# Performance work log

Measured on AMD Instinct MI355X. Metric: run time of the kernel, lower is better.

The kernel has to match this reference:

```python
import jax, jax.numpy as jnp
import numpy as np

B, C, H, W = 4, 256, 180, 180
N_BOX = 64


def _box_mask(gt_boxes, H, W):
    # gt_boxes: [B, N, 4] int32 = [lt_x, lt_y, rb_x, rb_y]
    # Original fills gt_mask[i, lt_y:rb_y, rb_x:lt_x] = 1 (x-slice is flipped).
    ys = jnp.arange(H)[:, None]            # [H,1]
    xs = jnp.arange(W)[None, :]            # [1,W]
    lt_x = gt_boxes[:, :, 0][:, :, None, None]
    lt_y = gt_boxes[:, :, 1][:, :, None, None]
    rb_x = gt_boxes[:, :, 2][:, :, None, None]
    rb_y = gt_boxes[:, :, 3][:, :, None, None]
    inside = (ys >= lt_y) & (ys < rb_y) & (xs >= rb_x) & (xs < lt_x)  # [B,N,H,W]
    return jnp.any(inside, axis=1)         # [B,H,W] bool


def setup_inputs() -> dict:
    key = jax.random.key(0)
    k1, k2, k3, k4, k5, k6 = jax.random.split(key, 6)
    inp = jax.random.normal(k1, (B, C, H, W), dtype=jnp.float32)
    tgt = jax.random.normal(k2, (B, C, H, W), dtype=jnp.float32)
    # Build boxes with flipped-x convention: lt_x > rb_x, lt_y < rb_y.
    x2 = jax.random.randint(k3, (B, N_BOX), 0, W - 50)
    bw = jax.random.randint(k4, (B, N_BOX), 5, 45)
    y1 = jax.random.randint(k5, (B, N_BOX), 0, H - 50)
    bh = jax.random.randint(k6, (B, N_BOX), 5, 45)
    gt_boxes = jnp.stack([x2 + bw, y1, x2, y1 + bh], axis=-1).astype(jnp.int32)
    return {"input": inp, "target": tgt, "gt_boxes": gt_boxes}


def reference(input, target, gt_boxes):
    b, c, h, w = input.shape
    mask = _box_mask(gt_boxes, h, w)                        # [B,H,W]
    x = jnp.transpose(input, (0, 2, 3, 1))                  # [B,H,W,C]
    t = jnp.transpose(target, (0, 2, 3, 1))
    positives = jnp.any(t != 0, axis=-1).astype(x.dtype) * mask.astype(x.dtype)
    pos_normalizer = jnp.sum(positives)
    reg_weights = positives / pos_normalizer                # [B,H,W]
    # masked weighted MSE; zero weights make non-positive pixels contribute 0,
    # matching the original's boolean-index gather.
    t = jnp.where(jnp.isnan(t), x, t)
    loss = 0.5 * (x - t) ** 2 * reg_weights[..., None]      # [B,H,W,C]
    imitation_loss = jnp.sum(jnp.mean(loss, axis=-1)) / b
    return imitation_loss
```

## Files before the change

### kernel.cpp

```cpp
#include <hip/hip_runtime.h>
#include <hip/hip_bf16.h>

#define B_     4
#define C_     256
#define H_     180
#define W_     180
#define NBOX   64
#define HW_    (H_ * W_)
#define GROUPS (HW_ / 4)
#define GTILES 32
#define PTILES 127
#define KCH    16
#define CPC    16
#define NBLK   (PTILES * B_)

#define WMASK_OFF 0
#define PSUM_OFF  (B_ * HW_)
#define PNZ_OFF   (PSUM_OFF + KCH * B_ * GROUPS * 16)
#define ACC_OFF   (PNZ_OFF + KCH * B_ * GROUPS * 4)
#define WS_NEED   (ACC_OFF + 8)

__global__ __launch_bounds__(256) void mfl_mask(
    const int* __restrict__ boxes,
    unsigned char* __restrict__ wmask)
{
    const int tid = threadIdx.x;
    const int bx  = blockIdx.x;
    const int b   = blockIdx.y;

    __shared__ int sbox[NBOX * 4];
    sbox[tid] = boxes[b * NBOX * 4 + tid];
    __syncthreads();

    const int hw = bx * 256 + tid;
    if (hw < HW_) {
        const int h = hw / W_, w = hw - (hw / W_) * W_;
        int msk = 0;
        #pragma unroll 8
        for (int n = 0; n < NBOX; ++n) {
            const int ltx = sbox[n * 4 + 0];
            const int lty = sbox[n * 4 + 1];
            const int rbx = sbox[n * 4 + 2];
            const int rby = sbox[n * 4 + 3];
            msk |= ((h >= lty) & (h < rby) & (w >= rbx) & (w < ltx));
        }
        wmask[b * HW_ + hw] = (unsigned char)msk;
    }
}

__global__ __launch_bounds__(256, 8) void mfl_stream(
    const float4* __restrict__ x4,
    const float4* __restrict__ t4,
    const unsigned char* __restrict__ wmask,
    float4* __restrict__ psum,
    unsigned int* __restrict__ pnz)
{
    const int g = blockIdx.x * 256 + threadIdx.x;
    if (g >= GROUPS) return;
    const int k = blockIdx.y;
    const int b = blockIdx.z;

    const uchar4 m4 = *(const uchar4*)(wmask + b * HW_ + 4 * g);
    if ((m4.x | m4.y | m4.z | m4.w) == 0) return;

    const size_t fbase = ((size_t)(b * C_ + k * CPC)) * GROUPS + g;
    const float4* xp = x4 + fbase;
    const float4* tp = t4 + fbase;

    float a0 = 0.f, a1 = 0.f, a2 = 0.f, a3 = 0.f;
    int   n0 = 0, n1 = 0, n2 = 0, n3 = 0;

    #pragma unroll 4
    for (int c = 0; c < CPC; ++c) {
        const float4 tv = tp[(size_t)c * GROUPS];
        const float4 xv = xp[(size_t)c * GROUPS];
        n0 |= (tv.x != 0.f); n1 |= (tv.y != 0.f);
        n2 |= (tv.z != 0.f); n3 |= (tv.w != 0.f);
        float d0 = xv.x - tv.x, d1 = xv.y - tv.y;
        float d2 = xv.z - tv.z, d3 = xv.w - tv.w;
        float s0 = 0.5f * d0 * d0, s1 = 0.5f * d1 * d1;
        float s2 = 0.5f * d2 * d2, s3 = 0.5f * d3 * d3;
        if (isnan(tv.x)) s0 = 0.f;  if (isnan(tv.y)) s1 = 0.f;
        if (isnan(tv.z)) s2 = 0.f;  if (isnan(tv.w)) s3 = 0.f;
        a0 += s0; a1 += s1; a2 += s2; a3 += s3;
    }

    const size_t o = ((size_t)(k * B_ + b)) * GROUPS + g;
    psum[o] = make_float4(a0, a1, a2, a3);
    pnz[o]  = (unsigned int)n0 | ((unsigned int)n1 << 8)
            | ((unsigned int)n2 << 16) | ((unsigned int)n3 << 24);
}

__global__ __launch_bounds__(256) void mfl_gate(
    const float* __restrict__ psumf,
    const unsigned char* __restrict__ pnzb,
    const unsigned char* __restrict__ wmask,
    float* __restrict__ ws_sum,
    unsigned int* __restrict__ ws_cnt)
{
    const int tid = threadIdx.x;
    const int bx  = blockIdx.x;
    const int b   = blockIdx.y;
    const int hw  = bx * 256 + tid;

    float s = 0.f;
    int   nz = 0, msk = 0;
    if (hw < HW_) {
        msk = wmask[b * HW_ + hw];
        if (msk) {
            const int g = hw >> 2, e = hw & 3;
            #pragma unroll
            for (int k = 0; k < KCH; ++k) {
                const size_t o = ((size_t)(k * B_ + b)) * GROUPS + g;
                s  += psumf[o * 4 + e];
                nz |= pnzb[o * 4 + e];
            }
        }
    }
    const bool ok = msk && nz;
    float sc = ok ? s : 0.f;
    int   cc = ok ? 1 : 0;

    #pragma unroll
    for (int off = 32; off > 0; off >>= 1) {
        sc += __shfl_down(sc, off, 64);
        cc += __shfl_down(cc, off, 64);
    }
    __shared__ float ws[4];
    __shared__ int   wc[4];
    if ((tid & 63) == 0) { ws[tid >> 6] = sc; wc[tid >> 6] = cc; }
    __syncthreads();
    if (tid == 0) {
        const float S  = ws[0] + ws[1] + ws[2] + ws[3];
        const int   Cn = wc[0] + wc[1] + wc[2] + wc[3];
        if (S != 0.f) atomicAdd(ws_sum, S);
        if (Cn != 0)  atomicAdd(ws_cnt, (unsigned int)Cn);
    }
}

__global__ void mfl_final(const float* ws_sum, const unsigned int* ws_cnt,
                          float* out)
{
    out[0] = ws_sum[0] / ((float)ws_cnt[0] * (float)C_ * (float)B_);
}

__global__ __launch_bounds__(256) void mfl_fallback(
    const float* __restrict__ x, const float* __restrict__ t,
    const int* __restrict__ boxes, float* ws_sum, unsigned int* ws_cnt)
{
    const int p = blockIdx.x * blockDim.x + threadIdx.x;
    float s = 0.0f; int cnt = 0;
    if (p < B_ * HW_) {
        const int b = p / HW_, hw = p - b * HW_;
        const int h = hw / W_, w = hw - h * W_;
        bool mask = false;
        const int* bb = boxes + b * NBOX * 4;
        for (int n = 0; n < NBOX; ++n) {
            mask |= ((h >= bb[n*4+1]) & (h < bb[n*4+3]) & (w >= bb[n*4+2]) & (w < bb[n*4+0]));
        }
        if (mask) {
            const float* xp = x + (size_t)b * C_ * HW_ + hw;
            const float* tp = t + (size_t)b * C_ * HW_ + hw;
            bool anynz = false;
            for (int c = 0; c < C_; ++c) {
                const float tv = tp[(size_t)c * HW_], xv = xp[(size_t)c * HW_];
                anynz |= (tv != 0.0f);
                const float d = xv - tv;
                float term = 0.5f * d * d;
                if (isnan(tv)) term = 0.0f;
                s += term;
            }
            if (anynz) cnt = 1; else s = 0.0f;
        }
    }
    for (int off = 32; off > 0; off >>= 1) {
        s += __shfl_down(s, off, 64); cnt += __shfl_down(cnt, off, 64);
    }
    __shared__ float ssum[4]; __shared__ int scnt[4];
    if ((threadIdx.x & 63) == 0) { ssum[threadIdx.x >> 6] = s; scnt[threadIdx.x >> 6] = cnt; }
    __syncthreads();
    if (threadIdx.x == 0) {
        const float S = ssum[0]+ssum[1]+ssum[2]+ssum[3];
        const int Cn = scnt[0]+scnt[1]+scnt[2]+scnt[3];
        if (S != 0.0f) atomicAdd(ws_sum, S);
        if (Cn != 0) atomicAdd(ws_cnt, (unsigned int)Cn);
    }
}

extern "C" void kernel_launch(void* const* d_in, const int* in_sizes, int n_in,
                              void* d_out, int out_size, void* d_ws, size_t ws_size,
                              hipStream_t stream)
{
    const float* x     = (const float*)d_in[0];
    const float* t     = (const float*)d_in[1];
    const int*   boxes = (const int*)d_in[2];
    float* out = (float*)d_out;
    char*  ws  = (char*)d_ws;

    if (ws_size < (size_t)WS_NEED) {
        float* ws_sum = (float*)ws;
        unsigned int* ws_cnt = (unsigned int*)(ws + 4);
        hipMemsetAsync(d_ws, 0, 8, stream);
        mfl_fallback<<<(B_ * HW_ + 255) / 256, 256, 0, stream>>>(x, t, boxes, ws_sum, ws_cnt);
        mfl_final<<<1, 1, 0, stream>>>(ws_sum, ws_cnt, out);
        return;
    }

    unsigned char* wmask  = (unsigned char*)(ws + WMASK_OFF);
    float4*        psum   = (float4*)(ws + PSUM_OFF);
    unsigned int*  pnz    = (unsigned int*)(ws + PNZ_OFF);
    float*         ws_sum = (float*)(ws + ACC_OFF);
    unsigned int*  ws_cnt = (unsigned int*)(ws + ACC_OFF + 4);

    hipMemsetAsync(ws + ACC_OFF, 0, 8, stream);

    dim3 gm(PTILES, B_);
    mfl_mask<<<gm, 256, 0, stream>>>(boxes, wmask);

    dim3 ga(GTILES, KCH, B_);
    mfl_stream<<<ga, 256, 0, stream>>>((const float4*)x, (const float4*)t,
                                       wmask, psum, pnz);

    dim3 gb(PTILES, B_);
    mfl_gate<<<gb, 256, 0, stream>>>((const float*)psum,
                                     (const unsigned char*)pnz,
                                     wmask, ws_sum, ws_cnt);

    mfl_final<<<1, 1, 0, stream>>>(ws_sum, ws_cnt, out);
}
```

Before: 61.98 us.

## Rewrite streaming kernel with batched loads and drop per-pixel mask skip

Replaces the streaming reduction kernel with one where each thread handles two float4 pixel groups and issues eight target and eight input loads per step before computing, with a scheduling barrier to keep the loads in flight together. The per-group mask check is removed, so every pixel is streamed. The channel split drops from 16 to 8 chunks, giving 32 channels per block, and the gate kernel sums fewer partials. The aim is more memory-level parallelism and fewer divergent early exits, at the cost of reading data under masked-out pixels that was skipped before.

Measured after the change: 69.57 us. +12.3%, slower.

```diff
diff --git a/kernel.cpp b/kernel.cpp
--- a/kernel.cpp
+++ b/kernel.cpp
@@ -8,11 +8,11 @@
 #define NBOX   64
 #define HW_    (H_ * W_)
 #define GROUPS (HW_ / 4)
-#define GTILES 32
+#define WGRP   512
+#define SEGS   ((GROUPS + WGRP - 1) / WGRP)
+#define KCH    8
+#define NC     (C_ / KCH)
 #define PTILES 127
-#define KCH    16
-#define CPC    16
-#define NBLK   (PTILES * B_)
 
 #define WMASK_OFF 0
 #define PSUM_OFF  (B_ * HW_)
@@ -48,47 +48,82 @@
     }
 }
 
-__global__ __launch_bounds__(256, 8) void mfl_stream(
+__global__ __launch_bounds__(256) void mfl_stream2(
     const float4* __restrict__ x4,
     const float4* __restrict__ t4,
-    const unsigned char* __restrict__ wmask,
     float4* __restrict__ psum,
     unsigned int* __restrict__ pnz)
 {
-    const int g = blockIdx.x * 256 + threadIdx.x;
-    if (g >= GROUPS) return;
-    const int k = blockIdx.y;
-    const int b = blockIdx.z;
-
-    const uchar4 m4 = *(const uchar4*)(wmask + b * HW_ + 4 * g);
-    if ((m4.x | m4.y | m4.z | m4.w) == 0) return;
-
-    const size_t fbase = ((size_t)(b * C_ + k * CPC)) * GROUPS + g;
-    const float4* xp = x4 + fbase;
-    const float4* tp = t4 + fbase;
-
-    float a0 = 0.f, a1 = 0.f, a2 = 0.f, a3 = 0.f;
-    int   n0 = 0, n1 = 0, n2 = 0, n3 = 0;
-
-    #pragma unroll 4
-    for (int c = 0; c < CPC; ++c) {
-        const float4 tv = tp[(size_t)c * GROUPS];
-        const float4 xv = xp[(size_t)c * GROUPS];
-        n0 |= (tv.x != 0.f); n1 |= (tv.y != 0.f);
-        n2 |= (tv.z != 0.f); n3 |= (tv.w != 0.f);
-        float d0 = xv.x - tv.x, d1 = xv.y - tv.y;
-        float d2 = xv.z - tv.z, d3 = xv.w - tv.w;
-        float s0 = 0.5f * d0 * d0, s1 = 0.5f * d1 * d1;
-        float s2 = 0.5f * d2 * d2, s3 = 0.5f * d3 * d3;
-        if (isnan(tv.x)) s0 = 0.f;  if (isnan(tv.y)) s1 = 0.f;
-        if (isnan(tv.z)) s2 = 0.f;  if (isnan(tv.w)) s3 = 0.f;
-        a0 += s0; a1 += s1; a2 += s2; a3 += s3;
-    }
-
-    const size_t o = ((size_t)(k * B_ + b)) * GROUPS + g;
-    psum[o] = make_float4(a0, a1, a2, a3);
-    pnz[o]  = (unsigned int)n0 | ((unsigned int)n1 << 8)
-            | ((unsigned int)n2 << 16) | ((unsigned int)n3 << 24);
+    const int tid  = threadIdx.x;
+    const int lane = tid & 63;
+    const int wid  = tid >> 6;
+    const int seg  = blockIdx.x;
+    const int k    = blockIdx.y;
+    const int b    = blockIdx.z;
+
+    const int g0 = seg * WGRP + wid * 128 + lane;
+    const int g1 = g0 + 64;
+    const bool v0 = g0 < GROUPS, v1 = g1 < GROUPS;
+    const int cg0 = v0 ? g0 : GROUPS - 1;
+    const int cg1 = v1 ? g1 : GROUPS - 1;
+
+    const size_t base = (size_t)(b * C_ + k * NC) * GROUPS;
+
+    float4 s0 = make_float4(0.f, 0.f, 0.f, 0.f);
+    float4 s1 = make_float4(0.f, 0.f, 0.f, 0.f);
+    float4 z0 = make_float4(0.f, 0.f, 0.f, 0.f);
+    float4 z1 = make_float4(0.f, 0.f, 0.f, 0.f);
+
+    for (int cb = 0; cb < NC; cb += 4) {
+        float4 T[8], X[8];
+        #pragma unroll
+        for (int j = 0; j < 4; ++j) {
+            const size_t rb = base + (size_t)(cb + j) * GROUPS;
+            T[2 * j]     = t4[rb + cg0];
+            T[2 * j + 1] = t4[rb + cg1];
+        }
+        #pragma unroll
+        for (int j = 0; j < 4; ++j) {
+            const size_t rb = base + (size_t)(cb + j) * GROUPS;
+            X[2 * j]     = x4[rb + cg0];
+            X[2 * j + 1] = x4[rb + cg1];
+        }
+        __builtin_amdgcn_sched_barrier(0);
+        #pragma unroll
+        for (int j = 0; j < 8; ++j) {
+            const float4 tv = T[j];
+            const float4 xv = X[j];
+            float4& s = (j & 1) ? s1 : s0;
+            float4& z = (j & 1) ? z1 : z0;
+            z.x += (tv.x != 0.f) ? 1.f : 0.f;
+            z.y += (tv.y != 0.f) ? 1.f : 0.f;
+            z.z += (tv.z != 0.f) ? 1.f : 0.f;
+            z.w += (tv.w != 0.f) ? 1.f : 0.f;
+            float d0 = xv.x - tv.x, d1 = xv.y - tv.y;
+            float d2 = xv.z - tv.z, d3 = xv.w - tv.w;
+            float m0 = 0.5f * d0 * d0, m1 = 0.5f * d1 * d1;
+            float m2 = 0.5f * d2 * d2, m3 = 0.5f * d3 * d3;
+            if (isnan(tv.x)) m0 = 0.f;  if (isnan(tv.y)) m1 = 0.f;
+            if (isnan(tv.z)) m2 = 0.f;  if (isnan(tv.w)) m3 = 0.f;
+            s.x += m0; s.y += m1; s.z += m2; s.w += m3;
+        }
+    }
+
+    const size_t o = (size_t)(k * B_ + b) * GROUPS;
+    if (v0) {
+        psum[o + g0] = s0;
+        pnz[o + g0] = (unsigned int)(z0.x > 0.f)
+                    | ((unsigned int)(z0.y > 0.f) << 8)
+                    | ((unsigned int)(z0.z > 0.f) << 16)
+                    | ((unsigned int)(z0.w > 0.f) << 24);
+    }
+    if (v1) {
+        psum[o + g1] = s1;
+        pnz[o + g1] = (unsigned int)(z1.x > 0.f)
+                    | ((unsigned int)(z1.y > 0.f) << 8)
+                    | ((unsigned int)(z1.z > 0.f) << 16)
+                    | ((unsigned int)(z1.w > 0.f) << 24);
+    }
 }
 
 __global__ __launch_bounds__(256) void mfl_gate(
@@ -217,9 +252,9 @@
     dim3 gm(PTILES, B_);
     mfl_mask<<<gm, 256, 0, stream>>>(boxes, wmask);
 
-    dim3 ga(GTILES, KCH, B_);
-    mfl_stream<<<ga, 256, 0, stream>>>((const float4*)x, (const float4*)t,
-                                       wmask, psum, pnz);
+    dim3 ga(SEGS, KCH, B_);
+    mfl_stream2<<<ga, 256, 0, stream>>>((const float4*)x, (const float4*)t,
+                                        psum, pnz);
 
     dim3 gb(PTILES, B_);
     mfl_gate<<<gb, 256, 0, stream>>>((const float*)psum,
```
